# Performance work log

Measured on AMD Instinct MI355X. Metric: run time of the kernel, lower is better.

Reference implementation:

```python
import jax, jax.numpy as jnp
import numpy as np

NUM_USER, NUM_ITEM, NUM_HIDDEN = 4096, 16384, 64
B, L = 1024, 50  # users in batch, items per user


def setup_inputs() -> dict:
    key = jax.random.key(0)
    k1, k2, k3, k4, k5 = jax.random.split(key, 5)
    return {
        "idx_user": jax.random.randint(k1, (B,), 0, NUM_USER),
        "item_sets": jax.random.randint(k2, (B, L), 0, NUM_ITEM),
        "rating_sets": jax.random.uniform(k3, (B, L), dtype=jnp.float32),
        "embed_user": 0.1 * jax.random.normal(k4, (NUM_USER, NUM_HIDDEN), dtype=jnp.float32),
        "embed_item": 0.1 * jax.random.normal(k5, (NUM_ITEM, NUM_HIDDEN), dtype=jnp.float32),
    }


def reference(idx_user, item_sets, rating_sets, embed_user, embed_item):
    # pred: [num_user, num_item] = U @ I^T
    pred = jnp.einsum("uh,ih->ui", embed_user, embed_item)
    # Vectorized scatter replacing the original nested Python loop:
    # rows broadcast to [B, L] so (row, col) pairs cover every rated entry.
    rows = idx_user[:, None]  # [B, 1] -> broadcasts against [B, L] items
    zeros = jnp.zeros((NUM_USER, NUM_ITEM), dtype=pred.dtype)
    mask = zeros.at[rows, item_sets].set(1.0)
    label = zeros.at[rows, item_sets].set(rating_sets)
    pred_mask = pred * mask
    sparsity = (NUM_USER * NUM_ITEM) / jnp.sum(mask)
    return pred_mask, label, sparsity
```

## Files before the change

kernel.cpp:

```cpp
#include <hip/hip_runtime.h>

#define NUM_USER   4096
#define NUM_ITEM   16384
#define NUM_HIDDEN 64
#define B_SZ       1024
#define L_SZ       50
#define NPAIR      (B_SZ * L_SZ)
#define SEG_ITEMS  1024
#define NSEG       (NUM_USER * (NUM_ITEM / SEG_ITEMS))
#define CAP        64
#define NBUCKET    1024

__global__ void pair_kernel(const int* __restrict__ idx_user,
                            const int* __restrict__ item_sets,
                            const float* __restrict__ rating_sets,
                            const float* __restrict__ embed_user,
                            const float* __restrict__ embed_item,
                            unsigned int* __restrict__ seg_count,
                            unsigned int* __restrict__ seg_key,
                            float* __restrict__ seg_val,
                            float* __restrict__ seg_rat) {
    const int p    = blockIdx.x * 4 + (threadIdx.x >> 6);
    const int lane = threadIdx.x & 63;
    if (p >= NPAIR) return;
    const int b  = p / L_SZ;
    const int u  = idx_user[b];
    const int it = item_sets[p];

    float v = embed_user[u * NUM_HIDDEN + lane] * embed_item[it * NUM_HIDDEN + lane];
    #pragma unroll
    for (int m = 32; m >= 1; m >>= 1) v += __shfl_xor(v, m, 64);

    if (lane == 0) {
        const int seg = u * (NUM_ITEM / SEG_ITEMS) + (it >> 10);
        unsigned int slot = atomicAdd(&seg_count[seg], 1u);
        if (slot < CAP) {
            const int base = seg * CAP + (int)slot;
            seg_key[base] = ((unsigned int)p << 10) | (unsigned int)(it & (SEG_ITEMS - 1));
            seg_val[base] = v;
            seg_rat[base] = rating_sets[p];
        }
    }
}

__global__ void fill_inject_kernel(const unsigned int* __restrict__ seg_count,
                                   const unsigned int* __restrict__ seg_key,
                                   const float* __restrict__ seg_val,
                                   const float* __restrict__ seg_rat,
                                   float* __restrict__ pred_mask,
                                   float* __restrict__ label,
                                   unsigned int* __restrict__ ucount) {
    const int seg = blockIdx.x;
    const int t   = threadIdx.x;
    const size_t cell = (size_t)seg * SEG_ITEMS + t * 4;

    float4 pv = {0.f, 0.f, 0.f, 0.f};
    float4 lv = {0.f, 0.f, 0.f, 0.f};

    unsigned int k = seg_count[seg];
    if (k > CAP) k = CAP;

    if (k > 0) {
        int bk0 = -1, bk1 = -1, bk2 = -1, bk3 = -1;
        int bi0 = 0,  bi1 = 0,  bi2 = 0,  bi3 = 0;
        const int base = seg * CAP;
        const int j0   = t * 4;
        for (int i = 0; i < (int)k; ++i) {
            const int key  = (int)seg_key[base + i];
            const int rel  = (key & (SEG_ITEMS - 1)) - j0;
            bool m0 = (rel == 0) && (key > bk0); bk0 = m0 ? key : bk0; bi0 = m0 ? i : bi0;
            bool m1 = (rel == 1) && (key > bk1); bk1 = m1 ? key : bk1; bi1 = m1 ? i : bi1;
            bool m2 = (rel == 2) && (key > bk2); bk2 = m2 ? key : bk2; bi2 = m2 ? i : bi2;
            bool m3 = (rel == 3) && (key > bk3); bk3 = m3 ? key : bk3; bi3 = m3 ? i : bi3;
        }
        if (bk0 >= 0) { pv.x = seg_val[base + bi0]; lv.x = seg_rat[base + bi0]; }
        if (bk1 >= 0) { pv.y = seg_val[base + bi1]; lv.y = seg_rat[base + bi1]; }
        if (bk2 >= 0) { pv.z = seg_val[base + bi2]; lv.z = seg_rat[base + bi2]; }
        if (bk3 >= 0) { pv.w = seg_val[base + bi3]; lv.w = seg_rat[base + bi3]; }

        unsigned int n = (bk0 >= 0) + (bk1 >= 0) + (bk2 >= 0) + (bk3 >= 0);
        #pragma unroll
        for (int m = 32; m >= 1; m >>= 1) n += __shfl_xor(n, m, 64);
        if ((t & 63) == 0 && n > 0)
            atomicAdd(&ucount[seg & (NBUCKET - 1)], n);
    }

    *(float4*)(pred_mask + cell) = pv;
    *(float4*)(label     + cell) = lv;
}

__global__ void sparsity_kernel(const unsigned int* __restrict__ ucount,
                                float* __restrict__ out) {
    __shared__ unsigned int warp_sum[4];
    const int t = threadIdx.x;
    unsigned int s = 0;
    #pragma unroll
    for (int i = 0; i < NBUCKET / 256; ++i) s += ucount[t + i * 256];
    #pragma unroll
    for (int m = 32; m >= 1; m >>= 1) s += __shfl_xor(s, m, 64);
    if ((t & 63) == 0) warp_sum[t >> 6] = s;
    __syncthreads();
    if (t == 0) {
        unsigned int total = warp_sum[0] + warp_sum[1] + warp_sum[2] + warp_sum[3];
        out[0] = (float)((double)NUM_USER * (double)NUM_ITEM / (double)total);
    }
}

extern "C" void kernel_launch(void* const* d_in, const int* in_sizes, int n_in,
                              void* d_out, int out_size, void* d_ws, size_t ws_size,
                              hipStream_t stream) {
    const int*   idx_user    = (const int*)d_in[0];
    const int*   item_sets   = (const int*)d_in[1];
    const float* rating_sets = (const float*)d_in[2];
    const float* embed_user  = (const float*)d_in[3];
    const float* embed_item  = (const float*)d_in[4];

    float* pred_mask = (float*)d_out;
    float* label     = pred_mask + (size_t)NUM_USER * NUM_ITEM;
    float* sparsity  = label     + (size_t)NUM_USER * NUM_ITEM;

    unsigned int* seg_count = (unsigned int*)d_ws;
    unsigned int* ucount    = seg_count + NSEG;
    unsigned int* seg_key   = ucount + NBUCKET;
    float*        seg_val   = (float*)(seg_key + (size_t)NSEG * CAP);
    float*        seg_rat   = seg_val + (size_t)NSEG * CAP;

    hipMemsetAsync(d_ws, 0, (size_t)(NSEG + NBUCKET) * sizeof(int), stream);

    pair_kernel<<<NPAIR / 4, 256, 0, stream>>>(idx_user, item_sets, rating_sets,
                                               embed_user, embed_item,
                                               seg_count, seg_key, seg_val, seg_rat);
    fill_inject_kernel<<<NSEG, 256, 0, stream>>>(seg_count, seg_key, seg_val, seg_rat,
                                                 pred_mask, label, ucount);
    sparsity_kernel<<<1, 256, 0, stream>>>(ucount, sparsity);
}
```

Before: 142.5 us.

## Use thread-per-pair dot products and persistent multi-segment fill blocks

The pair kernel now computes each dot product in a single thread with float4 loads, replacing the wave-per-pair shuffle reduction, and issues one atomic per thread. The fill kernel uses 2048 blocks, each looping over 32 segments, instead of one block per segment, so there are far fewer blocks to schedule and one ucount atomic per wave per block. In exchange, per-thread embedding reads are strided rather than coalesced across lanes, and each fill block has a long serial loop.

```diff
diff --git a/kernel.cpp b/kernel.cpp
--- a/kernel.cpp
+++ b/kernel.cpp
@@ -7,39 +7,43 @@
 #define L_SZ       50
 #define NPAIR      (B_SZ * L_SZ)
 #define SEG_ITEMS  1024
-#define NSEG       (NUM_USER * (NUM_ITEM / SEG_ITEMS))
+#define SEGS_PER_USER (NUM_ITEM / SEG_ITEMS)
+#define NSEG       (NUM_USER * SEGS_PER_USER)
 #define CAP        64
 #define NBUCKET    1024
+#define FILL_BLOCKS 2048
+#define SEGS_PER_BLOCK (NSEG / FILL_BLOCKS)
 
-__global__ void pair_kernel(const int* __restrict__ idx_user,
-                            const int* __restrict__ item_sets,
-                            const float* __restrict__ rating_sets,
-                            const float* __restrict__ embed_user,
-                            const float* __restrict__ embed_item,
-                            unsigned int* __restrict__ seg_count,
-                            unsigned int* __restrict__ seg_key,
-                            float* __restrict__ seg_val,
-                            float* __restrict__ seg_rat) {
-    const int p    = blockIdx.x * 4 + (threadIdx.x >> 6);
-    const int lane = threadIdx.x & 63;
-    if (p >= NPAIR) return;
+__global__ void pair_bin_kernel(const int* __restrict__ idx_user,
+                                const int* __restrict__ item_sets,
+                                const float* __restrict__ rating_sets,
+                                const float* __restrict__ embed_user,
+                                const float* __restrict__ embed_item,
+                                unsigned int* __restrict__ seg_count,
+                                unsigned int* __restrict__ seg_key,
+                                float* __restrict__ seg_val,
+                                float* __restrict__ seg_rat) {
+    const int p  = blockIdx.x * 256 + threadIdx.x;
     const int b  = p / L_SZ;
     const int u  = idx_user[b];
     const int it = item_sets[p];
 
-    float v = embed_user[u * NUM_HIDDEN + lane] * embed_item[it * NUM_HIDDEN + lane];
-    #pragma unroll
-    for (int m = 32; m >= 1; m >>= 1) v += __shfl_xor(v, m, 64);
+    const float4* eu = (const float4*)(embed_user + (size_t)u  * NUM_HIDDEN);
+    const float4* ei = (const float4*)(embed_item + (size_t)it * NUM_HIDDEN);
+    float acc = 0.f;
+    #pragma unroll 4
+    for (int j = 0; j < NUM_HIDDEN / 4; ++j) {
+        float4 a = eu[j], c = ei[j];
+        acc += a.x * c.x + a.y * c.y + a.z * c.z + a.w * c.w;
+    }
 
-    if (lane == 0) {
-        const int seg = u * (NUM_ITEM / SEG_ITEMS) + (it >> 10);
-        unsigned int slot = atomicAdd(&seg_count[seg], 1u);
-        if (slot < CAP) {
-            const int base = seg * CAP + (int)slot;
-            seg_key[base] = ((unsigned int)p << 10) | (unsigned int)(it & (SEG_ITEMS - 1));
-            seg_val[base] = v;
-            seg_rat[base] = rating_sets[p];
-        }
+    const int seg = (u << 4) | (it >> 10);
+    unsigned int slot = atomicAdd(&seg_count[seg], 1u);
+    if (slot < CAP) {
+        const int base = seg * CAP + (int)slot;
+        seg_key[base] = ((unsigned int)p << 10) | (unsigned int)(it & (SEG_ITEMS - 1));
+        seg_val[base] = acc;
+        seg_rat[base] = rating_sets[p];
     }
 }
 
@@ -47,46 +51,48 @@
                                    const unsigned int* __restrict__ seg_key,
                                    const float* __restrict__ seg_val,
                                    const float* __restrict__ seg_rat,
-                                   float* __restrict__ pred_mask,
-                                   float* __restrict__ label,
+                                   float4* __restrict__ pred4,
+                                   float4* __restrict__ label4,
                                    unsigned int* __restrict__ ucount) {
-    const int seg = blockIdx.x;
-    const int t   = threadIdx.x;
-    const size_t cell = (size_t)seg * SEG_ITEMS + t * 4;
+    const int t    = threadIdx.x;
+    const int seg0 = blockIdx.x * SEGS_PER_BLOCK;
+    const int j0   = t * 4;
+    unsigned int nmatch = 0;
 
-    float4 pv = {0.f, 0.f, 0.f, 0.f};
-    float4 lv = {0.f, 0.f, 0.f, 0.f};
+    for (int s = 0; s < SEGS_PER_BLOCK; ++s) {
+        const int seg = seg0 + s;
+        float4 pv = {0.f, 0.f, 0.f, 0.f};
+        float4 lv = {0.f, 0.f, 0.f, 0.f};
 
-    unsigned int k = seg_count[seg];
-    if (k > CAP) k = CAP;
+        unsigned int k = seg_count[seg];
+        if (k) {
+            if (k > CAP) k = CAP;
+            int bk0 = -1, bk1 = -1, bk2 = -1, bk3 = -1;
+            int bi0 = 0,  bi1 = 0,  bi2 = 0,  bi3 = 0;
+            const int base = seg * CAP;
+            for (int i = 0; i < (int)k; ++i) {
+                const int key = (int)seg_key[base + i];
+                const int rel = (key & (SEG_ITEMS - 1)) - j0;
+                bool m0 = (rel == 0) && (key > bk0); bk0 = m0 ? key : bk0; bi0 = m0 ? i : bi0;
+                bool m1 = (rel == 1) && (key > bk1); bk1 = m1 ? key : bk1; bi1 = m1 ? i : bi1;
+                bool m2 = (rel == 2) && (key > bk2); bk2 = m2 ? key : bk2; bi2 = m2 ? i : bi2;
+                bool m3 = (rel == 3) && (key > bk3); bk3 = m3 ? key : bk3; bi3 = m3 ? i : bi3;
+            }
+            if (bk0 >= 0) { pv.x = seg_val[base + bi0]; lv.x = seg_rat[base + bi0]; ++nmatch; }
+            if (bk1 >= 0) { pv.y = seg_val[base + bi1]; lv.y = seg_rat[base + bi1]; ++nmatch; }
+            if (bk2 >= 0) { pv.z = seg_val[base + bi2]; lv.z = seg_rat[base + bi2]; ++nmatch; }
+            if (bk3 >= 0) { pv.w = seg_val[base + bi3]; lv.w = seg_rat[base + bi3]; ++nmatch; }
+        }
 
-    if (k > 0) {
-        int bk0 = -1, bk1 = -1, bk2 = -1, bk3 = -1;
-        int bi0 = 0,  bi1 = 0,  bi2 = 0,  bi3 = 0;
-        const int base = seg * CAP;
-        const int j0   = t * 4;
-        for (int i = 0; i < (int)k; ++i) {
-            const int key  = (int)seg_key[base + i];
-            const int rel  = (key & (SEG_ITEMS - 1)) - j0;
-            bool m0 = (rel == 0) && (key > bk0); bk0 = m0 ? key : bk0; bi0 = m0 ? i : bi0;
-            bool m1 = (rel == 1) && (key > bk1); bk1 = m1 ? key : bk1; bi1 = m1 ? i : bi1;
-            bool m2 = (rel == 2) && (key > bk2); bk2 = m2 ? key : bk2; bi2 = m2 ? i : bi2;
-            bool m3 = (rel == 3) && (key > bk3); bk3 = m3 ? key : bk3; bi3 = m3 ? i : bi3;
-        }
-        if (bk0 >= 0) { pv.x = seg_val[base + bi0]; lv.x = seg_rat[base + bi0]; }
-        if (bk1 >= 0) { pv.y = seg_val[base + bi1]; lv.y = seg_rat[base + bi1]; }
-        if (bk2 >= 0) { pv.z = seg_val[base + bi2]; lv.z = seg_rat[base + bi2]; }
-        if (bk3 >= 0) { pv.w = seg_val[base + bi3]; lv.w = seg_rat[base + bi3]; }
-
-        unsigned int n = (bk0 >= 0) + (bk1 >= 0) + (bk2 >= 0) + (bk3 >= 0);
-        #pragma unroll
-        for (int m = 32; m >= 1; m >>= 1) n += __shfl_xor(n, m, 64);
-        if ((t & 63) == 0 && n > 0)
-            atomicAdd(&ucount[seg & (NBUCKET - 1)], n);
+        const size_t pos = (size_t)seg * (SEG_ITEMS / 4) + t;
+        pred4[pos]  = pv;
+        label4[pos] = lv;
     }
 
-    *(float4*)(pred_mask + cell) = pv;
-    *(float4*)(label     + cell) = lv;
+    #pragma unroll
+    for (int m = 32; m >= 1; m >>= 1) nmatch += __shfl_xor(nmatch, m, 64);
+    if ((t & 63) == 0 && nmatch)
+        atomicAdd(&ucount[blockIdx.x & (NBUCKET - 1)], nmatch);
 }
 
 __global__ void sparsity_kernel(const unsigned int* __restrict__ ucount,
@@ -127,10 +133,11 @@
 
     hipMemsetAsync(d_ws, 0, (size_t)(NSEG + NBUCKET) * sizeof(int), stream);
 
-    pair_kernel<<<NPAIR / 4, 256, 0, stream>>>(idx_user, item_sets, rating_sets,
-                                               embed_user, embed_item,
-                                               seg_count, seg_key, seg_val, seg_rat);
-    fill_inject_kernel<<<NSEG, 256, 0, stream>>>(seg_count, seg_key, seg_val, seg_rat,
-                                                 pred_mask, label, ucount);
+    pair_bin_kernel<<<NPAIR / 256, 256, 0, stream>>>(idx_user, item_sets, rating_sets,
+                                                     embed_user, embed_item,
+                                                     seg_count, seg_key, seg_val, seg_rat);
+    fill_inject_kernel<<<FILL_BLOCKS, 256, 0, stream>>>(seg_count, seg_key, seg_val, seg_rat,
+                                                        (float4*)pred_mask, (float4*)label,
+                                                        ucount);
     sparsity_kernel<<<1, 256, 0, stream>>>(ucount, sparsity);
 }
```

Measured after the change: 166.8 us, median of 3. 1.17x slower.
